# Kernel tuning notes

Measured on AMD Instinct MI355X. Metric: run time of the kernel, lower is better.

Reference implementation:

```python
import jax, jax.numpy as jnp
import numpy as np

H = 1024          # hidden_size
I = 4096          # intermediate_size
TAU = 9           # hashcode_len
LN_EPS = 1e-12    # layer_norm_eps


def setup_inputs() -> dict:
    key = jax.random.key(0)
    k1, k2, k3, k4 = jax.random.split(key, 4)
    return {
        "hidden_states": jax.random.normal(k1, (4, 2048, H), jnp.float32),
        "ln_weight": jnp.ones((H,), jnp.float32),
        "ln_bias": jnp.zeros((H,), jnp.float32),
        "k_weight": 0.02 * jax.random.normal(k2, (I, H), jnp.float32),
        "q_weight": 0.02 * jax.random.normal(k3, (I, H), jnp.float32),
        "bias": 0.001 * jax.random.normal(k4, (H,), jnp.float32),
    }


def _l2_normalize(x):
    # matches F.normalize(x, dim=-1): x / max(||x||, 1e-12)
    n = jnp.sqrt(jnp.sum(x * x, axis=-1, keepdims=True))
    return x / jnp.maximum(n, 1e-12)


def reference(hidden_states, ln_weight, ln_bias, k_weight, q_weight, bias):
    lead_shape = hidden_states.shape[:-1]
    x = hidden_states.reshape(-1, H)  # [N, H]

    # LayerNorm
    mu = jnp.mean(x, axis=-1, keepdims=True)
    var = jnp.mean(jnp.square(x - mu), axis=-1, keepdims=True)
    x = (x - mu) * jax.lax.rsqrt(var + LN_EPS) * ln_weight + ln_bias

    # YOSO expectation kernel: B_ij = (1 - arccos(<q_i, k_j>)/pi)^tau
    Q = _l2_normalize(x)         # [N, H]
    K = _l2_normalize(k_weight)  # [I, H]
    s = jnp.clip(jnp.einsum('nh,ih->ni', Q, K), -1.0 + 1e-6, 1.0 - 1e-6)
    B = jnp.power(1.0 - jnp.arccos(s) / jnp.pi, TAU)  # [N, I]

    X = jnp.einsum('ni,ih->nh', B, q_weight)  # V = q_weight
    X = _l2_normalize(X) + bias
    return X.reshape(*lead_shape, H)
```

## Files before the change

kernel.cpp:

```cpp
#include <hip/hip_runtime.h>

#define HD 1024
#define ID 4096
#define NR 8192

typedef float f32x4 __attribute__((ext_vector_type(4)));
typedef __bf16 bf16x8 __attribute__((ext_vector_type(8)));
typedef int i32x8 __attribute__((ext_vector_type(8)));

__device__ inline ushort f2bf(float f) {
    union { float f; unsigned u; } v; v.f = f;
    unsigned u = v.u;
    unsigned r = (u + 0x7fffu + ((u >> 16) & 1u)) >> 16;
    return (ushort)r;
}

__device__ inline float wave_sum(float v) {
#pragma unroll
    for (int o = 32; o > 0; o >>= 1) v += __shfl_xor(v, o, 64);
    return v;
}

template <int N> __device__ __forceinline__ void vmw() {
    static_assert(N >= 0 && N <= 4, "vmcnt");
    if constexpr (N == 0) asm volatile("s_waitcnt vmcnt(0)" ::: "memory");
    else if constexpr (N == 1) asm volatile("s_waitcnt vmcnt(1)" ::: "memory");
    else if constexpr (N == 2) asm volatile("s_waitcnt vmcnt(2)" ::: "memory");
    else if constexpr (N == 3) asm volatile("s_waitcnt vmcnt(3)" ::: "memory");
    else asm volatile("s_waitcnt vmcnt(4)" ::: "memory");
}
__device__ __forceinline__ void barrier_() {
    __builtin_amdgcn_sched_barrier(0);
    __builtin_amdgcn_s_barrier();
    __builtin_amdgcn_sched_barrier(0);
}
__device__ __forceinline__ void lgk0_() {
    asm volatile("s_waitcnt lgkmcnt(0)" ::: "memory");
    __builtin_amdgcn_sched_barrier(0);
}

__device__ __forceinline__ float yoso_act(float v) {
    float s = fminf(fmaxf(v, -0.999999f), 0.999999f);
    float a = fabsf(s);
    float p = 0.49998557f + a * (-0.06751706f + a * (0.02363794f - a * 0.00596170f));
    float q = sqrtf(1.0f - a) * p;
    float tt = (s >= 0.0f) ? 1.0f - q : q;
    float t2 = tt * tt, t4 = t2 * t2, t8 = t4 * t4;
    return t8 * tt;
}

__global__ __launch_bounds__(256, 3) void gemm1f_kernel(
    const unsigned char* __restrict__ Ap, const unsigned char* __restrict__ Bp,
    ushort* __restrict__ Cp, int N, int K) {
    __shared__ unsigned char la[128 * 128] __attribute__((aligned(16)));
    __shared__ unsigned char lb[128 * 128] __attribute__((aligned(16)));
    const int tid = threadIdx.x;
    const int w = tid >> 6, lane = tid & 63;
    const int bid = blockIdx.x;
    const int xcd = bid & 7, cu = (bid >> 3) & 31, rnd = bid >> 8;
    const int brow = (xcd * 8 + (cu >> 2)) * 128;
    const int bcol = (rnd * 4 + (cu & 3)) * 128;
    const int wr = (w >> 1) * 64;
    const int wc = (w & 1) * 64;
    f32x4 acc[4][4] = {};
    const int srow = lane >> 3;
    const int scolb = ((lane & 7) ^ (lane >> 3)) << 4;

    for (int k0 = 0; k0 < K; k0 += 128) {
#pragma unroll
        for (int it = 0; it < 4; ++it) {
            const int rb = w * 32 + it * 8;
            const unsigned char* ga = Ap + (size_t)(brow + rb + srow) * K + k0 + scolb;
            const unsigned char* gb = Bp + (size_t)(bcol + rb + srow) * K + k0 + scolb;
            __builtin_amdgcn_global_load_lds(
                (const __attribute__((address_space(1))) void*)ga,
                (__attribute__((address_space(3))) void*)&la[rb * 128], 16, 0, 0);
            __builtin_amdgcn_global_load_lds(
                (const __attribute__((address_space(1))) void*)gb,
                (__attribute__((address_space(3))) void*)&lb[rb * 128], 16, 0, 0);
        }
        __syncthreads();
        i32x8 af[4], bfr[4];
        const int base = (lane >> 4) << 5;
#pragma unroll
        for (int m = 0; m < 4; ++m) {
            const int row = wr + m * 16 + (lane & 15);
            const int key = (row & 7) << 4;
            const uint4 lo = *(const uint4*)(la + row * 128 + (base ^ key));
            const uint4 hi = *(const uint4*)(la + row * 128 + ((base + 16) ^ key));
            af[m] = (i32x8){(int)lo.x, (int)lo.y, (int)lo.z, (int)lo.w,
                            (int)hi.x, (int)hi.y, (int)hi.z, (int)hi.w};
        }
#pragma unroll
        for (int n = 0; n < 4; ++n) {
            const int row = wc + n * 16 + (lane & 15);
            const int key = (row & 7) << 4;
            const uint4 lo = *(const uint4*)(lb + row * 128 + (base ^ key));
            const uint4 hi = *(const uint4*)(lb + row * 128 + ((base + 16) ^ key));
            bfr[n] = (i32x8){(int)lo.x, (int)lo.y, (int)lo.z, (int)lo.w,
                             (int)hi.x, (int)hi.y, (int)hi.z, (int)hi.w};
        }
#pragma unroll
        for (int m = 0; m < 4; ++m)
#pragma unroll
            for (int n = 0; n < 4; ++n)
                acc[m][n] = __builtin_amdgcn_mfma_scale_f32_16x16x128_f8f6f4(
                    af[m], bfr[n], acc[m][n], 0, 0,
                    0, 0x7F7F7F7F, 0, 0x7F7F7F7F);
        __syncthreads();
    }
    const int crow0 = brow + wr + ((lane >> 4) << 2);
    const int ccol0 = bcol + wc + (lane & 15);
#pragma unroll
    for (int m = 0; m < 4; ++m)
#pragma unroll
        for (int n = 0; n < 4; ++n)
#pragma unroll
            for (int r = 0; r < 4; ++r) {
                int row = crow0 + m * 16 + r;
                int col = ccol0 + n * 16;
                Cp[(size_t)row * N + col] =
                    f2bf(yoso_act(acc[m][n][r] * 0.00390625f));
            }
}

template <int NW, int ACT>
__global__ __launch_bounds__(512, 2) void gemm8p_kernel(
    const ushort* __restrict__ Ap, const ushort* __restrict__ Bp,
    void* __restrict__ Cv, int N, int K, int nt) {
    __shared__ char lds[131072] __attribute__((aligned(16)));
    const int tid = threadIdx.x;
    const int w = tid >> 6, l = tid & 63;
    const int wm = w >> 2, wn = w & 3;
    const int bid = blockIdx.x;
    const int swz = (bid & 7) * ((int)gridDim.x >> 3) + (bid >> 3);
    const int brow = (swz & 31) * 256;
    const int bcol = (swz >> 5) * (128 * NW);
    const int colsw = ((l & 7) ^ (l >> 3)) << 4;

    f32x4 acc[8][2 * NW] = {};
    bf16x8 areg[4][2];
    bf16x8 breg[2][NW][2];

    auto sA = [&](int t, int mh) {
#pragma unroll
        for (int i = 0; i < 2; ++i) {
            int s = (w * 2 + i) * 8 + (l >> 3);
            int r = ((s >> 6) << 7) + mh * 64 + (s & 63);
            const char* src = (const char*)Ap + (((size_t)(brow + r) * K + t * 64) << 1) + colsw;
            __builtin_amdgcn_global_load_lds(
                (const __attribute__((address_space(1))) void*)src,
                (__attribute__((address_space(3))) void*)&lds[(t & 1) * 32768 + mh * 16384 +
                                                              (w * 2 + i) * 1024],
                16, 0, 0);
        }
    };
    auto sB = [&](int t, int nh) {
#pragma unroll
        for (int i = 0; i < NW; ++i) {
            constexpr int SH = (NW == 2) ? 5 : 4;
            int s = (w * NW + i) * 8 + (l >> 3);
            int r = ((s >> SH) << (SH + 1)) + nh * (16 * NW) + (s & (16 * NW - 1));
            const char* src = (const char*)Bp + (((size_t)(bcol + r) * K + t * 64) << 1) + colsw;
            __builtin_amdgcn_global_load_lds(
                (const __attribute__((address_space(1))) void*)src,
                (__attribute__((address_space(3))) void*)&lds[65536 + (t & 1) * (NW * 16384) +
                                                              nh * (NW * 8192) + (w * NW + i) * 1024],
                16, 0, 0);
        }
    };
    auto load_a = [&](int db, int mh) {
#pragma unroll
        for (int m = 0; m < 4; ++m)
#pragma unroll
            for (int ks = 0; ks < 2; ++ks) {
                int s = wm * 64 + m * 16 + (l & 15);
                areg[m][ks] = *(const bf16x8*)(lds + db * 32768 + mh * 16384 + s * 128 +
                                               ((ks * 64 + ((l >> 4) << 4)) ^ ((l & 7) << 4)));
            }
    };
    auto load_b = [&](int db, int nh) {
#pragma unroll
        for (int n = 0; n < NW; ++n)
#pragma unroll
            for (int ks = 0; ks < 2; ++ks) {
                int s = wn * (16 * NW) + n * 16 + (l & 15);
                breg[nh][n][ks] = *(const bf16x8*)(lds + 65536 + db * (NW * 16384) +
                                                   nh * (NW * 8192) + s * 128 +
                                                   ((ks * 64 + ((l >> 4) << 4)) ^ ((l & 7) << 4)));
            }
    };
    auto mma = [&](int mh, int nh) {
#pragma unroll
        for (int m = 0; m < 4; ++m)
#pragma unroll
            for (int n = 0; n < NW; ++n)
#pragma unroll
                for (int ks = 0; ks < 2; ++ks)
                    acc[mh * 4 + m][nh * NW + n] = __builtin_amdgcn_mfma_f32_16x16x32_bf16(
                        areg[m][ks], breg[nh][n][ks], acc[mh * 4 + m][nh * NW + n], 0, 0, 0);
    };

    sA(0, 0); sB(0, 0); sB(0, 1); sA(0, 1);
    vmw<3>();
    barrier_();

    for (int t = 0; t < nt; ++t) {
        const int db = t & 1;
        const bool more = (t + 1 < nt);
        load_a(db, 0); load_b(db, 0);
        if (more) sA(t + 1, 0);
        barrier_(); lgk0_();
        __builtin_amdgcn_s_setprio(1); mma(0, 0); __builtin_amdgcn_s_setprio(0);
        __builtin_amdgcn_sched_barrier(0);
        if (more) vmw<4>(); else vmw<2>();
        barrier_();
        load_b(db, 1);
        if (more) sB(t + 1, 0);
        barrier_(); lgk0_();
        __builtin_amdgcn_s_setprio(1); mma(0, 1); __builtin_amdgcn_s_setprio(0);
        __builtin_amdgcn_sched_barrier(0);
        if (more) vmw<3>(); else vmw<0>();
        barrier_();
        load_a(db, 1);
        if (more) sB(t + 1, 1);
        barrier_(); lgk0_();
        __builtin_amdgcn_s_setprio(1); mma(1, 1); __builtin_amdgcn_s_setprio(0);
        barrier_();
        if (more) sA(t + 1, 1);
        barrier_();
        __builtin_amdgcn_s_setprio(1); mma(1, 0); __builtin_amdgcn_s_setprio(0);
        __builtin_amdgcn_sched_barrier(0);
        if (more) vmw<3>();
        barrier_();
    }

    char* wsl = lds + w * 16384;
    constexpr int E = ACT ? 2 : 4;
    constexpr int BPR = NW * 32 * E;
    constexpr int LPR = BPR / 16;
    constexpr int RPI = 64 / LPR;
#pragma unroll
    for (int m = 0; m < 8; ++m)
#pragma unroll
        for (int n = 0; n < 2 * NW; ++n)
#pragma unroll
            for (int r = 0; r < 4; ++r) {
                int row = m * 16 + ((l >> 4) << 2) + r;
                int colb = (n * 16 + (l & 15)) * E;
                float v = acc[m][n][r];
                if (ACT) {
                    *(ushort*)(wsl + row * 128 + (colb ^ ((row & 7) << 4))) = f2bf(yoso_act(v));
                } else {
                    *(float*)(wsl + row * 128 + (colb ^ ((row & 7) << 4))) = v;
                }
            }
    asm volatile("s_waitcnt lgkmcnt(0)" ::: "memory");
#pragma unroll
    for (int it = 0; it < 2 * LPR; ++it) {
        int row = it * RPI + l / LPR;
        int cb = (l % LPR) * 16;
        uint4 d = *(const uint4*)(wsl + row * 128 + (cb ^ ((row & 7) << 4)));
        int grow = brow + wm * 128 + row;
        size_t off = ((size_t)grow * N + (bcol + wn * (NW * 32))) * E + cb;
        *(uint4*)((char*)Cv + off) = d;
    }
}

__global__ __launch_bounds__(256) void prep_kernel(
    const float* __restrict__ hs, const float* __restrict__ lnw,
    const float* __restrict__ lnb, const float* __restrict__ kw,
    const float* __restrict__ qw, unsigned char* __restrict__ Qf,
    unsigned char* __restrict__ Kf, ushort* __restrict__ VT) {
    __shared__ float smem[64][65];
    const int b = blockIdx.x, t = threadIdx.x;
    const int lane = t & 63, wid = t >> 6;
    if (b < NR) {
        const float4 v = reinterpret_cast<const float4*>(hs + (size_t)b * HD)[t];
        float s  = v.x + v.y + v.z + v.w;
        float ss = v.x*v.x + v.y*v.y + v.z*v.z + v.w*v.w;
        s = wave_sum(s); ss = wave_sum(ss);
        if (lane == 0) { smem[0][wid] = s; smem[1][wid] = ss; }
        __syncthreads();
        float st  = smem[0][0] + smem[0][1] + smem[0][2] + smem[0][3];
        float sst = smem[1][0] + smem[1][1] + smem[1][2] + smem[1][3];
        float mu   = st * (1.0f / HD);
        float var  = sst * (1.0f / HD) - mu * mu;
        float rstd = rsqrtf(var + 1e-12f);
        const float4 wv = reinterpret_cast<const float4*>(lnw)[t];
        const float4 bv = reinterpret_cast<const float4*>(lnb)[t];
        float y0 = (v.x - mu) * rstd * wv.x + bv.x;
        float y1 = (v.y - mu) * rstd * wv.y + bv.y;
        float y2 = (v.z - mu) * rstd * wv.z + bv.z;
        float y3 = (v.w - mu) * rstd * wv.w + bv.w;
        float n2 = wave_sum(y0*y0 + y1*y1 + y2*y2 + y3*y3);
        if (lane == 0) smem[2][wid] = n2;
        __syncthreads();
        float nt2 = smem[2][0] + smem[2][1] + smem[2][2] + smem[2][3];
        float sc = 16.0f / fmaxf(sqrtf(nt2), 1e-12f);
        int r = __builtin_amdgcn_cvt_pk_fp8_f32(y0 * sc, y1 * sc, 0, false);
        r = __builtin_amdgcn_cvt_pk_fp8_f32(y2 * sc, y3 * sc, r, true);
        reinterpret_cast<int*>(Qf + (size_t)b * HD)[t] = r;
    } else if (b < NR + ID) {
        const int row = b - NR;
        const float4 v = reinterpret_cast<const float4*>(kw + (size_t)row * HD)[t];
        float n2 = wave_sum(v.x*v.x + v.y*v.y + v.z*v.z + v.w*v.w);
        if (lane == 0) smem[0][wid] = n2;
        __syncthreads();
        float nt2 = smem[0][0] + smem[0][1] + smem[0][2] + smem[0][3];
        float sc = 16.0f / fmaxf(sqrtf(nt2), 1e-12f);
        int r = __builtin_amdgcn_cvt_pk_fp8_f32(v.x * sc, v.y * sc, 0, false);
        r = __builtin_amdgcn_cvt_pk_fp8_f32(v.z * sc, v.w * sc, r, true);
        reinterpret_cast<int*>(Kf + (size_t)row * HD)[t] = r;
    } else {
        const int b2 = b - NR - ID;
        const int bi = (b2 & 63) * 64, bh = (b2 >> 6) * 64;
        const int r0 = t >> 4, c0 = (t & 15) << 2;
#pragma unroll
        for (int rr = 0; rr < 64; rr += 16) {
            float4 val = *reinterpret_cast<const float4*>(
                &qw[(size_t)(bi + rr + r0) * HD + bh + c0]);
            smem[rr + r0][c0 + 0] = val.x; smem[rr + r0][c0 + 1] = val.y;
            smem[rr + r0][c0 + 2] = val.z; smem[rr + r0][c0 + 3] = val.w;
        }
        __syncthreads();
#pragma unroll
        for (int rr = 0; rr < 64; rr += 16) {
            ushort4 o;
            o.x = f2bf(smem[c0 + 0][rr + r0]);
            o.y = f2bf(smem[c0 + 1][rr + r0]);
            o.z = f2bf(smem[c0 + 2][rr + r0]);
            o.w = f2bf(smem[c0 + 3][rr + r0]);
            *reinterpret_cast<ushort4*>(&VT[(size_t)(bh + rr + r0) * ID + bi + c0]) = o;
        }
    }
}

__global__ __launch_bounds__(256) void outnorm_kernel(
    float* __restrict__ X, const float* __restrict__ bias) {
    __shared__ float red2[4];
    const int row = blockIdx.x, t = threadIdx.x;
    const int lane = t & 63, wid = t >> 6;
    float4 v = reinterpret_cast<float4*>(X + (size_t)row * HD)[t];
    float n2 = wave_sum(v.x*v.x + v.y*v.y + v.z*v.z + v.w*v.w);
    if (lane == 0) red2[wid] = n2;
    __syncthreads();
    float nt = red2[0] + red2[1] + red2[2] + red2[3];
    float sc = 1.0f / fmaxf(sqrtf(nt), 1e-12f);
    const float4 bv = reinterpret_cast<const float4*>(bias)[t];
    float4 o;
    o.x = v.x * sc + bv.x; o.y = v.y * sc + bv.y;
    o.z = v.z * sc + bv.z; o.w = v.w * sc + bv.w;
    reinterpret_cast<float4*>(X + (size_t)row * HD)[t] = o;
}

extern "C" void kernel_launch(void* const* d_in, const int* in_sizes, int n_in,
                              void* d_out, int out_size, void* d_ws, size_t ws_size,
                              hipStream_t stream) {
    const float* hs   = (const float*)d_in[0];
    const float* lnw  = (const float*)d_in[1];
    const float* lnb  = (const float*)d_in[2];
    const float* kw   = (const float*)d_in[3];
    const float* qw   = (const float*)d_in[4];
    const float* bias = (const float*)d_in[5];
    float* out = (float*)d_out;

    char* ws = (char*)d_ws;
    unsigned char* Qf = (unsigned char*)(ws);
    unsigned char* Kf = (unsigned char*)(ws + (size_t)8388608);
    ushort* VT   = (ushort*)(ws + (size_t)12582912);
    ushort* Bmat = (ushort*)(ws + (size_t)20971520);

    prep_kernel<<<NR + ID + 1024, 256, 0, stream>>>(hs, lnw, lnb, kw, qw, Qf, Kf, VT);
    gemm1f_kernel<<<(NR / 128) * (ID / 128), 256, 0, stream>>>(
        Qf, Kf, Bmat, ID, HD);
    gemm8p_kernel<1, 0><<<(NR / 256) * (HD / 128), 512, 0, stream>>>(
        Bmat, VT, (void*)out, HD, ID, ID / 64);
    outnorm_kernel<<<NR, 256, 0, stream>>>(out, bias);
}
```

Before: 170.4 us.

## Replace pipelined second GEMM with simple single-buffered K=128 tiled kernel

Replaces the hand-scheduled double-buffered gemm8p kernel (with staged prefetch, setprio and vmcnt waits) with a simpler kernel that stages a 256x128 A tile and 128x128 B tile per K=128 step into a single LDS buffer, synchronises, then runs MFMAs. Block-to-tile mapping changes to an XCD-aware layout, and the epilogue writes fp32 results directly instead of going through LDS. This removes barrier overhead and halves the number of K iterations, but loses overlap of global loads with compute and makes the output stores uncoalesced.

New measurement: 167.2 us. No clear change (-1.8%).

```diff
diff --git a/kernel.cpp b/kernel.cpp
--- a/kernel.cpp
+++ b/kernel.cpp
@@ -19,24 +19,6 @@
 #pragma unroll
     for (int o = 32; o > 0; o >>= 1) v += __shfl_xor(v, o, 64);
     return v;
-}
-
-template <int N> __device__ __forceinline__ void vmw() {
-    static_assert(N >= 0 && N <= 4, "vmcnt");
-    if constexpr (N == 0) asm volatile("s_waitcnt vmcnt(0)" ::: "memory");
-    else if constexpr (N == 1) asm volatile("s_waitcnt vmcnt(1)" ::: "memory");
-    else if constexpr (N == 2) asm volatile("s_waitcnt vmcnt(2)" ::: "memory");
-    else if constexpr (N == 3) asm volatile("s_waitcnt vmcnt(3)" ::: "memory");
-    else asm volatile("s_waitcnt vmcnt(4)" ::: "memory");
-}
-__device__ __forceinline__ void barrier_() {
-    __builtin_amdgcn_sched_barrier(0);
-    __builtin_amdgcn_s_barrier();
-    __builtin_amdgcn_sched_barrier(0);
-}
-__device__ __forceinline__ void lgk0_() {
-    asm volatile("s_waitcnt lgkmcnt(0)" ::: "memory");
-    __builtin_amdgcn_sched_barrier(0);
 }
 
 __device__ __forceinline__ float yoso_act(float v) {
@@ -124,147 +106,83 @@
             }
 }
 
-template <int NW, int ACT>
-__global__ __launch_bounds__(512, 2) void gemm8p_kernel(
+__global__ __launch_bounds__(512) void gemm2k_kernel(
     const ushort* __restrict__ Ap, const ushort* __restrict__ Bp,
-    void* __restrict__ Cv, int N, int K, int nt) {
-    __shared__ char lds[131072] __attribute__((aligned(16)));
+    float* __restrict__ Cv, int N, int K, int nt) {
+    __shared__ char lds[98304] __attribute__((aligned(16)));
     const int tid = threadIdx.x;
-    const int w = tid >> 6, l = tid & 63;
-    const int wm = w >> 2, wn = w & 3;
+    const int w = tid >> 6, lane = tid & 63;
+    const int wm = w >> 1, wn = w & 1;
     const int bid = blockIdx.x;
-    const int swz = (bid & 7) * ((int)gridDim.x >> 3) + (bid >> 3);
-    const int brow = (swz & 31) * 256;
-    const int bcol = (swz >> 5) * (128 * NW);
-    const int colsw = ((l & 7) ^ (l >> 3)) << 4;
-
-    f32x4 acc[8][2 * NW] = {};
-    bf16x8 areg[4][2];
-    bf16x8 breg[2][NW][2];
-
-    auto sA = [&](int t, int mh) {
-#pragma unroll
-        for (int i = 0; i < 2; ++i) {
-            int s = (w * 2 + i) * 8 + (l >> 3);
-            int r = ((s >> 6) << 7) + mh * 64 + (s & 63);
-            const char* src = (const char*)Ap + (((size_t)(brow + r) * K + t * 64) << 1) + colsw;
+    const int xcd = bid & 7, cu = bid >> 3;
+    const int brow = (xcd * 4 + (cu >> 3)) * 256;
+    const int bcol = (cu & 7) * 128;
+    const int strow = tid >> 4;
+    const int sslot = (tid & 15) ^ (strow & 15);
+    const int scolb = sslot << 4;
+
+    f32x4 acc[4][4] = {};
+
+    auto stage = [&](int t) {
+#pragma unroll
+        for (int u = 0; u < 8; ++u) {
+            int grow = brow + u * 32 + strow;
+            const char* src = (const char*)Ap + ((size_t)grow * K + t * 128) * 2 + scolb;
             __builtin_amdgcn_global_load_lds(
                 (const __attribute__((address_space(1))) void*)src,
-                (__attribute__((address_space(3))) void*)&lds[(t & 1) * 32768 + mh * 16384 +
-                                                              (w * 2 + i) * 1024],
+                (__attribute__((address_space(3))) void*)&lds[u * 8192 + tid * 16], 16, 0, 0);
+        }
+#pragma unroll
+        for (int u = 0; u < 4; ++u) {
+            int grow = bcol + u * 32 + strow;
+            const char* src = (const char*)Bp + ((size_t)grow * K + t * 128) * 2 + scolb;
+            __builtin_amdgcn_global_load_lds(
+                (const __attribute__((address_space(1))) void*)src,
+                (__attribute__((address_space(3))) void*)&lds[65536 + u * 8192 + tid * 16],
                 16, 0, 0);
         }
     };
-    auto sB = [&](int t, int nh) {
-#pragma unroll
-        for (int i = 0; i < NW; ++i) {
-            constexpr int SH = (NW == 2) ? 5 : 4;
-            int s = (w * NW + i) * 8 + (l >> 3);
-            int r = ((s >> SH) << (SH + 1)) + nh * (16 * NW) + (s & (16 * NW - 1));
-            const char* src = (const char*)Bp + (((size_t)(bcol + r) * K + t * 64) << 1) + colsw;
-            __builtin_amdgcn_global_load_lds(
-                (const __attribute__((address_space(1))) void*)src,
-                (__attribute__((address_space(3))) void*)&lds[65536 + (t & 1) * (NW * 16384) +
-                                                              nh * (NW * 8192) + (w * NW + i) * 1024],
-                16, 0, 0);
-        }
-    };
-    auto load_a = [&](int db, int mh) {
-#pragma unroll
-        for (int m = 0; m < 4; ++m)
-#pragma unroll
-            for (int ks = 0; ks < 2; ++ks) {
-                int s = wm * 64 + m * 16 + (l & 15);
-                areg[m][ks] = *(const bf16x8*)(lds + db * 32768 + mh * 16384 + s * 128 +
-                                               ((ks * 64 + ((l >> 4) << 4)) ^ ((l & 7) << 4)));
-            }
-    };
-    auto load_b = [&](int db, int nh) {
-#pragma unroll
-        for (int n = 0; n < NW; ++n)
-#pragma unroll
-            for (int ks = 0; ks < 2; ++ks) {
-                int s = wn * (16 * NW) + n * 16 + (l & 15);
-                breg[nh][n][ks] = *(const bf16x8*)(lds + 65536 + db * (NW * 16384) +
-                                                   nh * (NW * 8192) + s * 128 +
-                                                   ((ks * 64 + ((l >> 4) << 4)) ^ ((l & 7) << 4)));
-            }
-    };
-    auto mma = [&](int mh, int nh) {
-#pragma unroll
-        for (int m = 0; m < 4; ++m)
-#pragma unroll
-            for (int n = 0; n < NW; ++n)
-#pragma unroll
-                for (int ks = 0; ks < 2; ++ks)
-                    acc[mh * 4 + m][nh * NW + n] = __builtin_amdgcn_mfma_f32_16x16x32_bf16(
-                        areg[m][ks], breg[nh][n][ks], acc[mh * 4 + m][nh * NW + n], 0, 0, 0);
-    };
-
-    sA(0, 0); sB(0, 0); sB(0, 1); sA(0, 1);
-    vmw<3>();
-    barrier_();
 
     for (int t = 0; t < nt; ++t) {
-        const int db = t & 1;
-        const bool more = (t + 1 < nt);
-        load_a(db, 0); load_b(db, 0);
-        if (more) sA(t + 1, 0);
-        barrier_(); lgk0_();
-        __builtin_amdgcn_s_setprio(1); mma(0, 0); __builtin_amdgcn_s_setprio(0);
-        __builtin_amdgcn_sched_barrier(0);
-        if (more) vmw<4>(); else vmw<2>();
-        barrier_();
-        load_b(db, 1);
-        if (more) sB(t + 1, 0);
-        barrier_(); lgk0_();
-        __builtin_amdgcn_s_setprio(1); mma(0, 1); __builtin_amdgcn_s_setprio(0);
-        __builtin_amdgcn_sched_barrier(0);
-        if (more) vmw<3>(); else vmw<0>();
-        barrier_();
-        load_a(db, 1);
-        if (more) sB(t + 1, 1);
-        barrier_(); lgk0_();
-        __builtin_amdgcn_s_setprio(1); mma(1, 1); __builtin_amdgcn_s_setprio(0);
-        barrier_();
-        if (more) sA(t + 1, 1);
-        barrier_();
-        __builtin_amdgcn_s_setprio(1); mma(1, 0); __builtin_amdgcn_s_setprio(0);
-        __builtin_amdgcn_sched_barrier(0);
-        if (more) vmw<3>();
-        barrier_();
+        stage(t);
+        __syncthreads();
+#pragma unroll
+        for (int ks = 0; ks < 4; ++ks) {
+            bf16x8 af[4], bfr[4];
+            const int ckey = lane & 15;
+            const int chunk = ks * 4 + (lane >> 4);
+#pragma unroll
+            for (int m = 0; m < 4; ++m) {
+                int row = wm * 64 + m * 16 + (lane & 15);
+                af[m] = *(const bf16x8*)(lds + row * 256 + ((chunk ^ ckey) << 4));
+            }
+#pragma unroll
+            for (int n = 0; n < 4; ++n) {
+                int row = wn * 64 + n * 16 + (lane & 15);
+                bfr[n] = *(const bf16x8*)(lds + 65536 + row * 256 + ((chunk ^ ckey) << 4));
+            }
+#pragma unroll
+            for (int m = 0; m < 4; ++m)
+#pragma unroll
+                for (int n = 0; n < 4; ++n)
+                    acc[m][n] = __builtin_amdgcn_mfma_f32_16x16x32_bf16(
+                        af[m], bfr[n], acc[m][n], 0, 0, 0);
+        }
+        __syncthreads();
     }
 
-    char* wsl = lds + w * 16384;
-    constexpr int E = ACT ? 2 : 4;
-    constexpr int BPR = NW * 32 * E;
-    constexpr int LPR = BPR / 16;
-    constexpr int RPI = 64 / LPR;
-#pragma unroll
-    for (int m = 0; m < 8; ++m)
-#pragma unroll
-        for (int n = 0; n < 2 * NW; ++n)
+    const int crow0 = brow + wm * 64 + ((lane >> 4) << 2);
+    const int ccol0 = bcol + wn * 64 + (lane & 15);
+#pragma unroll
+    for (int m = 0; m < 4; ++m)
+#pragma unroll
+        for (int n = 0; n < 4; ++n)
 #pragma unroll
             for (int r = 0; r < 4; ++r) {
-                int row = m * 16 + ((l >> 4) << 2) + r;
-                int colb = (n * 16 + (l & 15)) * E;
-                float v = acc[m][n][r];
-                if (ACT) {
-                    *(ushort*)(wsl + row * 128 + (colb ^ ((row & 7) << 4))) = f2bf(yoso_act(v));
-                } else {
-                    *(float*)(wsl + row * 128 + (colb ^ ((row & 7) << 4))) = v;
-                }
-            }
-    asm volatile("s_waitcnt lgkmcnt(0)" ::: "memory");
-#pragma unroll
-    for (int it = 0; it < 2 * LPR; ++it) {
-        int row = it * RPI + l / LPR;
-        int cb = (l % LPR) * 16;
-        uint4 d = *(const uint4*)(wsl + row * 128 + (cb ^ ((row & 7) << 4)));
-        int grow = brow + wm * 128 + row;
-        size_t off = ((size_t)grow * N + (bcol + wn * (NW * 32))) * E + cb;
-        *(uint4*)((char*)Cv + off) = d;
-    }
+                int row = crow0 + m * 16 + r;
+                int col = ccol0 + n * 16;
+                Cv[(size_t)row * N + col] = acc[m][n][r];
+            }
 }
 
 __global__ __launch_bounds__(256) void prep_kernel(
@@ -374,7 +292,7 @@
     prep_kernel<<<NR + ID + 1024, 256, 0, stream>>>(hs, lnw, lnb, kw, qw, Qf, Kf, VT);
     gemm1f_kernel<<<(NR / 128) * (ID / 128), 256, 0, stream>>>(
         Qf, Kf, Bmat, ID, HD);
-    gemm8p_kernel<1, 0><<<(NR / 256) * (HD / 128), 512, 0, stream>>>(
-        Bmat, VT, (void*)out, HD, ID, ID / 64);
+    gemm2k_kernel<<<(NR / 256) * (HD / 128), 512, 0, stream>>>(
+        Bmat, VT, out, HD, ID, ID / 128);
     outnorm_kernel<<<NR, 256, 0, stream>>>(out, bias);
 }
```
